# Performance work log

Measured on AMD Instinct MI355X. Metric: run time of the kernel, lower is better.

The kernel has to match this reference:

```python
import jax, jax.numpy as jnp
import numpy as np

B, N, C, H, BS = 4, 4096, 1024, 16, 64
E = C // H          # head dim = 64
EPS = 1e-3

def setup_inputs() -> dict:
    key = jax.random.key(0)
    k0, k1, k2, k3 = jax.random.split(key, 4)
    x = jax.random.normal(k0, (B, N, C), jnp.float32)
    qkv_w = jax.random.normal(k1, (3 * C, C), jnp.float32) * 0.02
    proj_w = jax.random.normal(k2, (C, C), jnp.float32) * 0.02
    proj_b = jax.random.normal(k3, (C,), jnp.float32) * 0.02
    return {"x": x, "qkv_w": qkv_w, "proj_w": proj_w, "proj_b": proj_b}

def reference(x, qkv_w, proj_w, proj_b):
    b, n, c = x.shape
    h, e, bs = H, E, BS
    u = n // bs  # number of buckets
    # qkv projection (no bias), split to (B,H,N,e) per q/k/v
    qkv = (x @ qkv_w.T).reshape(b, n, 3, h, e).transpose(2, 0, 3, 1, 4)
    q, k, v = qkv[0], qkv[1], qkv[2]
    # feature maps: softmax(q) scaled, exp(k)
    q = jax.nn.softmax(q, axis=-1) * (e ** -0.5)
    k = jnp.exp(k)
    # bucket along sequence: (B,H,U,BS,e)
    b_q = q.reshape(b, h, u, bs, e)
    b_k = k.reshape(b, h, u, bs, e)
    b_v = v.reshape(b, h, u, bs, e)
    # per-bucket k sums and inter-bucket cumulative sums
    b_k_cumsum = jnp.cumsum(b_k.sum(axis=-2), axis=-2)            # (B,H,U,e)
    context = jnp.einsum('bhund,bhune->bhude', b_k, b_v)          # (B,H,U,e,e)
    context = jnp.cumsum(context, axis=2)
    # exclusive shift by one bucket (bucket_size > 1 path in original)
    context = jnp.concatenate(
        [jnp.zeros_like(context[:, :, :1]), context[:, :, :-1]], axis=2)
    b_k_cumsum = jnp.concatenate(
        [jnp.zeros_like(b_k_cumsum[:, :, :1]), b_k_cumsum[:, :, :-1]], axis=2)
    # normalizer, clamped from below at eps
    D_inv = 1.0 / jnp.maximum(
        jnp.einsum('bhud,bhund->bhun', b_k_cumsum, b_q), EPS)
    attn = jnp.einsum('bhund,bhude,bhun->bhune', b_q, context, D_inv)
    out = attn.reshape(b, h, n, e).transpose(0, 2, 1, 3).reshape(b, n, c)
    # output projection (dropouts are identity at eval)
    return out @ proj_w.T + proj_b
```

## Files before the change

kernel.cpp:

```cpp
#include <hip/hip_runtime.h>
#include <stdint.h>


typedef unsigned short u16;
typedef unsigned int u32;
typedef u16   u16x4  __attribute__((ext_vector_type(4)));
typedef u16   u16x8  __attribute__((ext_vector_type(8)));
typedef float f32x4  __attribute__((ext_vector_type(4)));
typedef float float4v __attribute__((ext_vector_type(4)));
typedef __bf16 bf16x8 __attribute__((ext_vector_type(8)));

__device__ __forceinline__ u16 f2bf(float f) {
  return __builtin_bit_cast(u16, (__bf16)f);
}
__device__ __forceinline__ float bf2f(u16 h) {
  return (float)__builtin_bit_cast(__bf16, h);
}

__device__ __forceinline__ void stage16(const u16* g, u16* l) {
  __builtin_amdgcn_global_load_lds(
      (const __attribute__((address_space(1))) u32*)g,
      (__attribute__((address_space(3))) u32*)l, 16, 0, 0);
}

__global__ __launch_bounds__(256) void cvt_all(
    const float* __restrict__ x, const float* __restrict__ wqf,
    const float* __restrict__ wpf, u16* __restrict__ xb,
    u16* __restrict__ wq, u16* __restrict__ wp) {
  int i = blockIdx.x * 256 + threadIdx.x;
  const float* in; u16* out; int j;
  if (i < 4194304)      { in = x;   out = xb; j = i; }
  else if (i < 4980736) { in = wqf; out = wq; j = i - 4194304; }
  else                  { in = wpf; out = wp; j = i - 4980736; }
  float4v v = reinterpret_cast<const float4v*>(in)[j];
  u16x4 o;
  o.x = f2bf(v.x); o.y = f2bf(v.y); o.z = f2bf(v.z); o.w = f2bf(v.w);
  reinterpret_cast<u16x4*>(out)[j] = o;
}

template <int EPI>
__global__ __launch_bounds__(512, 2) void gemm256(
    const u16* __restrict__ A,
    const u16* __restrict__ B,
    const float* __restrict__ bias,
    float* __restrict__ Cf,
    u16* __restrict__ Qf, u16* __restrict__ Kr, u16* __restrict__ Vr,
    int N, int K, int NT) {
  __shared__ u16 As[2][2][256][32];
  __shared__ u16 Bs[2][2][256][32];
  const int tid = threadIdx.x, lane = tid & 63, wave = tid >> 6;
  const int wm = wave >> 2, wn = wave & 3;
  const int l15 = lane & 15, l4 = lane >> 4;
  const int ntn = N >> 8;
  const int cpx = gridDim.x >> 3;
  const int bid = (blockIdx.x & 7) * cpx + (blockIdx.x >> 3);
  const int bm = bid / ntn, bn = bid % ntn;

  const int srow = tid >> 2;
  const int gsl8 = ((tid & 3) ^ ((tid >> 3) & 3)) * 8;
  const u16* Ag = A + (size_t)(bm * 256 + srow) * K + gsl8;
  const u16* Bg = B + (size_t)(bn * 256 + srow) * K + gsl8;
  const size_t rj = (size_t)128 * K;

  const int slotr = (l4 ^ ((l15 >> 1) & 3)) * 8;

  f32x4 acc[8][4] = {};
  bf16x8 a0, a1, a2, a3, a4, a5, a6, a7, b0, b1, b2, b3;

#define STG(P, buf, kh, kt)                                        \
  { const u16* g_ = P##g + (kt) + (kh) * 32;                       \
    stage16(g_,      &P##s[buf][kh][wave * 16][0]);                \
    stage16(g_ + rj, &P##s[buf][kh][128 + wave * 16][0]); }

#define LDA(r0_, r1_, r2_, r3_, kk, mh)                                  \
  { const u16* p_ = &As[cur][kk][wm * 128 + (mh) * 64 + l15][0] + slotr; \
    r0_ = *(const bf16x8*)(p_);                                          \
    r1_ = *(const bf16x8*)(p_ + 512);                                    \
    r2_ = *(const bf16x8*)(p_ + 1024);                                   \
    r3_ = *(const bf16x8*)(p_ + 1536); }

#define LDB(kk)                                                    \
  { const u16* p_ = &Bs[cur][kk][wn * 64 + l15][0] + slotr;        \
    b0 = *(const bf16x8*)(p_);                                     \
    b1 = *(const bf16x8*)(p_ + 512);                               \
    b2 = *(const bf16x8*)(p_ + 1024);                              \
    b3 = *(const bf16x8*)(p_ + 1536); }

#define MM(x, y, z) z = __builtin_amdgcn_mfma_f32_16x16x32_bf16(x, y, z, 0, 0, 0)
#define MFMA16(mb, x0, x1, x2, x3)                                 \
  __builtin_amdgcn_s_setprio(1);                                   \
  MM(x0, b0, acc[(mb) + 0][0]); MM(x0, b1, acc[(mb) + 0][1]);      \
  MM(x0, b2, acc[(mb) + 0][2]); MM(x0, b3, acc[(mb) + 0][3]);      \
  MM(x1, b0, acc[(mb) + 1][0]); MM(x1, b1, acc[(mb) + 1][1]);      \
  MM(x1, b2, acc[(mb) + 1][2]); MM(x1, b3, acc[(mb) + 1][3]);      \
  MM(x2, b0, acc[(mb) + 2][0]); MM(x2, b1, acc[(mb) + 2][1]);      \
  MM(x2, b2, acc[(mb) + 2][2]); MM(x2, b3, acc[(mb) + 2][3]);      \
  MM(x3, b0, acc[(mb) + 3][0]); MM(x3, b1, acc[(mb) + 3][1]);      \
  MM(x3, b2, acc[(mb) + 3][2]); MM(x3, b3, acc[(mb) + 3][3]);      \
  __builtin_amdgcn_s_setprio(0);

#define BARF()                                                     \
  { asm volatile("" ::: "memory");                                 \
    __builtin_amdgcn_s_barrier();                                  \
    asm volatile("" ::: "memory"); }

  STG(A, 0, 0, 0) STG(B, 0, 0, 0) STG(A, 0, 1, 0) STG(B, 0, 1, 0)
  asm volatile("s_waitcnt vmcnt(0)" ::: "memory");
  __builtin_amdgcn_s_barrier();
  asm volatile("" ::: "memory");

  for (int t = 0; t < NT; ++t) {
    const int cur = t & 1, nxt = cur ^ 1;
    const int ktn = (t + 1) << 6;
    const bool pre = (t + 1 < NT);
    LDB(0)
    LDA(a0, a1, a2, a3, 0, 0)
    LDA(a4, a5, a6, a7, 0, 1)
    if (pre) STG(A, nxt, 0, ktn)
    MFMA16(0, a0, a1, a2, a3)
    if (pre) STG(B, nxt, 0, ktn)
    MFMA16(4, a4, a5, a6, a7)
    if (pre) { asm volatile("s_waitcnt vmcnt(4)" ::: "memory"); }
    else     { asm volatile("s_waitcnt vmcnt(0)" ::: "memory"); }
    BARF()
    LDB(1)
    LDA(a0, a1, a2, a3, 1, 0)
    LDA(a4, a5, a6, a7, 1, 1)
    if (pre) STG(A, nxt, 1, ktn)
    MFMA16(0, a0, a1, a2, a3)
    if (pre) STG(B, nxt, 1, ktn)
    MFMA16(4, a4, a5, a6, a7)
    if (pre) { asm volatile("s_waitcnt vmcnt(4)" ::: "memory"); }
    BARF()
  }
#undef STG
#undef LDA
#undef LDB
#undef MM
#undef MFMA16
#undef BARF

  const int row0 = bm * 256 + wm * 128 + l4 * 4;
  const int col0 = bn * 256 + wn * 64 + l15;
  if constexpr (EPI == 0) {
    float bv[4];
#pragma unroll
    for (int ni = 0; ni < 4; ++ni) bv[ni] = bias[col0 + ni * 16];
#pragma unroll
    for (int mi = 0; mi < 8; ++mi)
#pragma unroll
      for (int i = 0; i < 4; ++i) {
        size_t r = (size_t)(row0 + mi * 16 + i) * N;
#pragma unroll
        for (int ni = 0; ni < 4; ++ni)
          Cf[r + col0 + ni * 16] = acc[mi][ni][i] + bv[ni];
      }
  } else {
    const int i3 = bn >> 2;
    const int h  = ((bn & 3) << 2) + wn;
    u16* dst = (i3 == 0) ? Qf : (i3 == 1 ? Kr : Vr);
#pragma unroll
    for (int mi = 0; mi < 8; ++mi)
#pragma unroll
      for (int i = 0; i < 4; ++i) {
        const int row = row0 + mi * 16 + i;
        const int bb = row >> 12, uu = (row >> 6) & 63, nn = row & 63;
        u16* op = dst + ((size_t)((bb * 16 + h) * 64 + uu)) * 4096
                      + nn * 64 + l15;
        float v0 = acc[mi][0][i], v1 = acc[mi][1][i];
        float v2 = acc[mi][2][i], v3 = acc[mi][3][i];
        if (i3 == 0) {
          float mx = fmaxf(fmaxf(v0, v1), fmaxf(v2, v3));
          mx = fmaxf(mx, __shfl_xor(mx, 1));
          mx = fmaxf(mx, __shfl_xor(mx, 2));
          mx = fmaxf(mx, __shfl_xor(mx, 4));
          mx = fmaxf(mx, __shfl_xor(mx, 8));
          float e0 = __expf(v0 - mx), e1 = __expf(v1 - mx);
          float e2 = __expf(v2 - mx), e3 = __expf(v3 - mx);
          float s = e0 + e1 + e2 + e3;
          s += __shfl_xor(s, 1); s += __shfl_xor(s, 2);
          s += __shfl_xor(s, 4); s += __shfl_xor(s, 8);
          float inv = 0.125f / s;
          op[0]  = f2bf(e0 * inv); op[16] = f2bf(e1 * inv);
          op[32] = f2bf(e2 * inv); op[48] = f2bf(e3 * inv);
        } else if (i3 == 1) {
          op[0]  = f2bf(__expf(v0)); op[16] = f2bf(__expf(v1));
          op[32] = f2bf(__expf(v2)); op[48] = f2bf(__expf(v3));
        } else {
          op[0]  = f2bf(v0); op[16] = f2bf(v1);
          op[32] = f2bf(v2); op[48] = f2bf(v3);
        }
      }
  }
}

__global__ __launch_bounds__(256) void buildctx(
    const u16* __restrict__ Kr,
    const u16* __restrict__ Vr,
    u16* __restrict__ ctxb, float* __restrict__ ksum) {
  const int bid = blockIdx.x;
  const int tid = threadIdx.x, lane = tid & 63, wave = tid >> 6;
  const int l15 = lane & 15, l4 = lane >> 4;
  __shared__ float ts[64][65];
  __shared__ u16 KtL[64][72];
  __shared__ u16 VtL[64][72];
  __shared__ float dp[64][4];

  const size_t base = (size_t)bid * 4096;

  {
    int n = tid >> 2, c = tid & 3;
    const u16* kp = Kr + base + n * 64 + c * 16;
#pragma unroll
    for (int j = 0; j < 16; ++j) ts[n][c * 16 + j] = bf2f(kp[j]);
  }
  __syncthreads();
  {
    int d = tid >> 2, c = tid & 3;
    u16x8 o0, o1;
#pragma unroll
    for (int j = 0; j < 8; ++j) o0[j] = f2bf(ts[c * 16 + j][d]);
#pragma unroll
    for (int j = 0; j < 8; ++j) o1[j] = f2bf(ts[c * 16 + 8 + j][d]);
    *reinterpret_cast<u16x8*>(&KtL[d][c * 16])     = o0;
    *reinterpret_cast<u16x8*>(&KtL[d][c * 16 + 8]) = o1;
  }
  __syncthreads();
  {
    int d = tid & 63, q = tid >> 6;
    float a = 0.f;
#pragma unroll
    for (int j = 0; j < 16; ++j) a += bf2f(KtL[d][q * 16 + j]);
    dp[d][q] = a;
  }
  {
    int n = tid >> 2, c = tid & 3;
    const u16* vp = Vr + base + n * 64 + c * 16;
#pragma unroll
    for (int j = 0; j < 16; ++j) ts[n][c * 16 + j] = bf2f(vp[j]);
  }
  __syncthreads();
  if (tid < 64)
    ksum[(size_t)bid * 64 + tid] = dp[tid][0] + dp[tid][1] + dp[tid][2] + dp[tid][3];
  {
    int e = tid >> 2, c = tid & 3;
    u16x8 o0, o1;
#pragma unroll
    for (int j = 0; j < 8; ++j) o0[j] = f2bf(ts[c * 16 + j][e]);
#pragma unroll
    for (int j = 0; j < 8; ++j) o1[j] = f2bf(ts[c * 16 + 8 + j][e]);
    *reinterpret_cast<u16x8*>(&VtL[e][c * 16])     = o0;
    *reinterpret_cast<u16x8*>(&VtL[e][c * 16 + 8]) = o1;
  }
  __syncthreads();

  f32x4 acc[4] = {};
#pragma unroll
  for (int kk = 0; kk < 2; ++kk) {
    bf16x8 av = *reinterpret_cast<const bf16x8*>(&VtL[wave * 16 + l15][kk * 32 + l4 * 8]);
#pragma unroll
    for (int ni = 0; ni < 4; ++ni) {
      bf16x8 bk = *reinterpret_cast<const bf16x8*>(&KtL[ni * 16 + l15][kk * 32 + l4 * 8]);
      acc[ni] = __builtin_amdgcn_mfma_f32_16x16x32_bf16(av, bk, acc[ni], 0, 0, 0);
    }
  }
  u16* cb = ctxb + base;
#pragma unroll
  for (int ni = 0; ni < 4; ++ni)
#pragma unroll
    for (int i = 0; i < 4; ++i)
      cb[(wave * 16 + l4 * 4 + i) * 64 + ni * 16 + l15] = f2bf(acc[ni][i]);
}

__global__ __launch_bounds__(256) void scanctx(
    u16* __restrict__ ctxb, float* __restrict__ ksum) {
  const int bh = blockIdx.x >> 2, c = blockIdx.x & 3;
  const int tid = threadIdx.x;
  u16* p = ctxb + (size_t)bh * 64 * 4096 + c * 1024 + tid * 4;
  float* kp = ksum + (size_t)bh * 64 * 64 + tid;
  const bool dok = (c == 0) && (tid < 64);

  float r0 = 0.f, r1 = 0.f, r2 = 0.f, r3 = 0.f, runk = 0.f;
#define LC(i) (*reinterpret_cast<const u16x4*>(p + (size_t)(i) * 4096))
#define LK(i) (dok ? kp[(size_t)(i) * 64] : 0.f)
  u16x4 c0 = LC(0), c1 = LC(1), c2 = LC(2), c3 = LC(3);
  float k0 = LK(0), k1 = LK(1), k2 = LK(2), k3 = LK(3);
  for (int u = 0; u < 64; u += 4) {
    const int i4 = u + 4 < 64 ? u + 4 : 63, i5 = u + 5 < 64 ? u + 5 : 63;
    const int i6 = u + 6 < 64 ? u + 6 : 63, i7 = u + 7 < 64 ? u + 7 : 63;
    u16x4 n0 = LC(i4), n1 = LC(i5), n2 = LC(i6), n3 = LC(i7);
    float m0 = LK(i4), m1 = LK(i5), m2 = LK(i6), m3 = LK(i7);
#define STEP(idx, cv, kv)                                                  \
    {                                                                      \
      u16x4 o;                                                             \
      o.x = f2bf(r0); o.y = f2bf(r1); o.z = f2bf(r2); o.w = f2bf(r3);      \
      *reinterpret_cast<u16x4*>(p + (size_t)(idx) * 4096) = o;             \
      if (dok) kp[(size_t)(idx) * 64] = runk;                              \
      r0 += bf2f(cv.x); r1 += bf2f(cv.y); r2 += bf2f(cv.z);                \
      r3 += bf2f(cv.w); runk += kv;                                        \
    }
    STEP(u, c0, k0) STEP(u + 1, c1, k1) STEP(u + 2, c2, k2) STEP(u + 3, c3, k3)
#undef STEP
    c0 = n0; c1 = n1; c2 = n2; c3 = n3;
    k0 = m0; k1 = m1; k2 = m2; k3 = m3;
  }
#undef LC
#undef LK
}

__global__ __launch_bounds__(256) void apply(
    const u16* __restrict__ Q, const u16* __restrict__ ctxc,
    const float* __restrict__ kcum, u16* __restrict__ AT) {
  const int bid = blockIdx.x;
  const int u = bid & 63, bh = bid >> 6, b = bh >> 4, h = bh & 15;
  const int tid = threadIdx.x, lane = tid & 63, wave = tid >> 6;
  const int l15 = lane & 15, l4 = lane >> 4;
  __shared__ float kc[64];
  __shared__ float dp[64][4];
  __shared__ float dinv[64];

  const size_t base = (size_t)bid * 4096;
  const u16* Qu = Q + base;
  if (tid < 64) kc[tid] = kcum[(size_t)bid * 64 + tid];
  __syncthreads();
  {
    int n = tid & 63, q = tid >> 6;
    const u16* qp = Qu + n * 64 + q * 16;
    float a = 0.f;
#pragma unroll
    for (int j = 0; j < 16; ++j) a += bf2f(qp[j]) * kc[q * 16 + j];
    dp[n][q] = a;
  }
  __syncthreads();
  if (tid < 64)
    dinv[tid] = 1.f / fmaxf(dp[tid][0] + dp[tid][1] + dp[tid][2] + dp[tid][3], 1e-3f);
  __syncthreads();

  f32x4 acc[4] = {};
  const u16* Cu = ctxc + base;
#pragma unroll
  for (int kk = 0; kk < 2; ++kk) {
    bf16x8 aq = *reinterpret_cast<const bf16x8*>(Qu + (wave * 16 + l15) * 64 + kk * 32 + l4 * 8);
#pragma unroll
    for (int ni = 0; ni < 4; ++ni) {
      bf16x8 bc = *reinterpret_cast<const bf16x8*>(Cu + (ni * 16 + l15) * 64 + kk * 32 + l4 * 8);
      acc[ni] = __builtin_amdgcn_mfma_f32_16x16x32_bf16(aq, bc, acc[ni], 0, 0, 0);
    }
  }
  const size_t orow = ((size_t)b * 4096 + u * 64 + wave * 16 + l4 * 4) * 1024 + h * 64;
#pragma unroll
  for (int i = 0; i < 4; ++i) {
    float di = dinv[wave * 16 + l4 * 4 + i];
#pragma unroll
    for (int ni = 0; ni < 4; ++ni)
      AT[orow + (size_t)i * 1024 + ni * 16 + l15] = f2bf(acc[ni][i] * di);
  }
}

extern "C" void kernel_launch(void* const* d_in, const int* in_sizes, int n_in,
                              void* d_out, int out_size, void* d_ws, size_t ws_size,
                              hipStream_t stream) {
  (void)in_sizes; (void)n_in; (void)out_size; (void)ws_size;
  const float* x      = (const float*)d_in[0];
  const float* qkv_w  = (const float*)d_in[1];
  const float* proj_w = (const float*)d_in[2];
  const float* proj_b = (const float*)d_in[3];
  float* out = (float*)d_out;

  char* ws = (char*)d_ws;
  u16* xb    = (u16*)(ws);
  u16* wq    = (u16*)(ws + 33554432);
  u16* wp    = (u16*)(ws + 39845888);
  u16* Qf    = (u16*)(ws + 41943040);
  u16* Kr    = (u16*)(ws + 75497472);
  u16* Vr    = (u16*)(ws + 109051904);
  u16* ctxb  = (u16*)(ws + 142606336);
  float* ksum = (float*)(ws + 176160768);
  u16* AT    = Kr;

  cvt_all<<<dim3(20480), dim3(256), 0, stream>>>(x, qkv_w, proj_w, xb, wq, wp);

  gemm256<2><<<dim3(64 * 12), dim3(512), 0, stream>>>(
      xb, wq, nullptr, nullptr, Qf, Kr, Vr, 3072, 1024, 16);
  buildctx<<<dim3(4096), dim3(256), 0, stream>>>(Kr, Vr, ctxb, ksum);
  scanctx<<<dim3(256), dim3(256), 0, stream>>>(ctxb, ksum);
  apply<<<dim3(4096), dim3(256), 0, stream>>>(Qf, ctxb, ksum, AT);
  gemm256<0><<<dim3(64 * 4), dim3(512), 0, stream>>>(
      AT, wp, proj_b, out, nullptr, nullptr, nullptr, 1024, 1024, 16);
}
```

Measured before the change: 244.9 us.

## Write K and V transposed from QKV GEMM epilogue, drop LDS transposes in buildctx

The QKV GEMM epilogue now stores exp(K) and V per bucket in a transposed (d-major) layout, with each lane writing four consecutive sequence positions as one 8-byte store. buildctx then reads MFMA operands and key sums straight from global memory, with no LDS staging, transposes or the extra barriers that went with them. The cost moves into the epilogue, whose stores are now strided by 64 elements across lanes and may coalesce less well than the earlier row-major writes.

```diff
diff --git a/kernel.cpp b/kernel.cpp
--- a/kernel.cpp
+++ b/kernel.cpp
@@ -44,7 +44,7 @@
     const u16* __restrict__ B,
     const float* __restrict__ bias,
     float* __restrict__ Cf,
-    u16* __restrict__ Qf, u16* __restrict__ Kr, u16* __restrict__ Vr,
+    u16* __restrict__ Qf, u16* __restrict__ Kt, u16* __restrict__ Vt,
     int N, int K, int NT) {
   __shared__ u16 As[2][2][256][32];
   __shared__ u16 Bs[2][2][256][32];
@@ -158,18 +158,17 @@
   } else {
     const int i3 = bn >> 2;
     const int h  = ((bn & 3) << 2) + wn;
-    u16* dst = (i3 == 0) ? Qf : (i3 == 1 ? Kr : Vr);
-#pragma unroll
-    for (int mi = 0; mi < 8; ++mi)
-#pragma unroll
-      for (int i = 0; i < 4; ++i) {
-        const int row = row0 + mi * 16 + i;
-        const int bb = row >> 12, uu = (row >> 6) & 63, nn = row & 63;
-        u16* op = dst + ((size_t)((bb * 16 + h) * 64 + uu)) * 4096
-                      + nn * 64 + l15;
-        float v0 = acc[mi][0][i], v1 = acc[mi][1][i];
-        float v2 = acc[mi][2][i], v3 = acc[mi][3][i];
-        if (i3 == 0) {
+    if (i3 == 0) {
+#pragma unroll
+      for (int mi = 0; mi < 8; ++mi)
+#pragma unroll
+        for (int i = 0; i < 4; ++i) {
+          const int row = row0 + mi * 16 + i;
+          const int bb = row >> 12, uu = (row >> 6) & 63, nn = row & 63;
+          u16* op = Qf + ((size_t)((bb * 16 + h) * 64 + uu)) * 4096
+                        + nn * 64 + l15;
+          float v0 = acc[mi][0][i], v1 = acc[mi][1][i];
+          float v2 = acc[mi][2][i], v3 = acc[mi][3][i];
           float mx = fmaxf(fmaxf(v0, v1), fmaxf(v2, v3));
           mx = fmaxf(mx, __shfl_xor(mx, 1));
           mx = fmaxf(mx, __shfl_xor(mx, 2));
@@ -183,87 +182,68 @@
           float inv = 0.125f / s;
           op[0]  = f2bf(e0 * inv); op[16] = f2bf(e1 * inv);
           op[32] = f2bf(e2 * inv); op[48] = f2bf(e3 * inv);
-        } else if (i3 == 1) {
-          op[0]  = f2bf(__expf(v0)); op[16] = f2bf(__expf(v1));
-          op[32] = f2bf(__expf(v2)); op[48] = f2bf(__expf(v3));
-        } else {
-          op[0]  = f2bf(v0); op[16] = f2bf(v1);
-          op[32] = f2bf(v2); op[48] = f2bf(v3);
+        }
+    } else {
+      u16* dst = (i3 == 1) ? Kt : Vt;
+#pragma unroll
+      for (int mi = 0; mi < 8; ++mi) {
+        const int row = row0 + mi * 16;
+        const int bb = row >> 12, uu = (row >> 6) & 63, nn = row & 63;
+        u16* op = dst + ((size_t)((bb * 16 + h) * 64 + uu)) * 4096 + nn;
+#pragma unroll
+        for (int ni = 0; ni < 4; ++ni) {
+          const int d = ni * 16 + l15;
+          u16x4 o;
+          if (i3 == 1) {
+            o.x = f2bf(__expf(acc[mi][ni][0]));
+            o.y = f2bf(__expf(acc[mi][ni][1]));
+            o.z = f2bf(__expf(acc[mi][ni][2]));
+            o.w = f2bf(__expf(acc[mi][ni][3]));
+          } else {
+            o.x = f2bf(acc[mi][ni][0]); o.y = f2bf(acc[mi][ni][1]);
+            o.z = f2bf(acc[mi][ni][2]); o.w = f2bf(acc[mi][ni][3]);
+          }
+          *reinterpret_cast<u16x4*>(op + d * 64) = o;
         }
       }
+    }
   }
 }
 
 __global__ __launch_bounds__(256) void buildctx(
-    const u16* __restrict__ Kr,
-    const u16* __restrict__ Vr,
+    const u16* __restrict__ Kt,
+    const u16* __restrict__ Vt,
     u16* __restrict__ ctxb, float* __restrict__ ksum) {
   const int bid = blockIdx.x;
   const int tid = threadIdx.x, lane = tid & 63, wave = tid >> 6;
   const int l15 = lane & 15, l4 = lane >> 4;
-  __shared__ float ts[64][65];
-  __shared__ u16 KtL[64][72];
-  __shared__ u16 VtL[64][72];
   __shared__ float dp[64][4];
-
   const size_t base = (size_t)bid * 4096;
 
-  {
-    int n = tid >> 2, c = tid & 3;
-    const u16* kp = Kr + base + n * 64 + c * 16;
-#pragma unroll
-    for (int j = 0; j < 16; ++j) ts[n][c * 16 + j] = bf2f(kp[j]);
-  }
-  __syncthreads();
   {
     int d = tid >> 2, c = tid & 3;
-    u16x8 o0, o1;
-#pragma unroll
-    for (int j = 0; j < 8; ++j) o0[j] = f2bf(ts[c * 16 + j][d]);
-#pragma unroll
-    for (int j = 0; j < 8; ++j) o1[j] = f2bf(ts[c * 16 + 8 + j][d]);
-    *reinterpret_cast<u16x8*>(&KtL[d][c * 16])     = o0;
-    *reinterpret_cast<u16x8*>(&KtL[d][c * 16 + 8]) = o1;
-  }
-  __syncthreads();
-  {
-    int d = tid & 63, q = tid >> 6;
+    const u16* kp = Kt + base + d * 64 + c * 16;
     float a = 0.f;
 #pragma unroll
-    for (int j = 0; j < 16; ++j) a += bf2f(KtL[d][q * 16 + j]);
-    dp[d][q] = a;
-  }
-  {
-    int n = tid >> 2, c = tid & 3;
-    const u16* vp = Vr + base + n * 64 + c * 16;
-#pragma unroll
-    for (int j = 0; j < 16; ++j) ts[n][c * 16 + j] = bf2f(vp[j]);
+    for (int j = 0; j < 16; ++j) a += bf2f(kp[j]);
+    dp[d][c] = a;
+  }
+
+  f32x4 acc[4] = {};
+#pragma unroll
+  for (int kk = 0; kk < 2; ++kk) {
+    bf16x8 av = *reinterpret_cast<const bf16x8*>(
+        Vt + base + (wave * 16 + l15) * 64 + kk * 32 + l4 * 8);
+#pragma unroll
+    for (int ni = 0; ni < 4; ++ni) {
+      bf16x8 bk = *reinterpret_cast<const bf16x8*>(
+          Kt + base + (ni * 16 + l15) * 64 + kk * 32 + l4 * 8);
+      acc[ni] = __builtin_amdgcn_mfma_f32_16x16x32_bf16(av, bk, acc[ni], 0, 0, 0);
+    }
   }
   __syncthreads();
   if (tid < 64)
     ksum[(size_t)bid * 64 + tid] = dp[tid][0] + dp[tid][1] + dp[tid][2] + dp[tid][3];
-  {
-    int e = tid >> 2, c = tid & 3;
-    u16x8 o0, o1;
-#pragma unroll
-    for (int j = 0; j < 8; ++j) o0[j] = f2bf(ts[c * 16 + j][e]);
-#pragma unroll
-    for (int j = 0; j < 8; ++j) o1[j] = f2bf(ts[c * 16 + 8 + j][e]);
-    *reinterpret_cast<u16x8*>(&VtL[e][c * 16])     = o0;
-    *reinterpret_cast<u16x8*>(&VtL[e][c * 16 + 8]) = o1;
-  }
-  __syncthreads();
-
-  f32x4 acc[4] = {};
-#pragma unroll
-  for (int kk = 0; kk < 2; ++kk) {
-    bf16x8 av = *reinterpret_cast<const bf16x8*>(&VtL[wave * 16 + l15][kk * 32 + l4 * 8]);
-#pragma unroll
-    for (int ni = 0; ni < 4; ++ni) {
-      bf16x8 bk = *reinterpret_cast<const bf16x8*>(&KtL[ni * 16 + l15][kk * 32 + l4 * 8]);
-      acc[ni] = __builtin_amdgcn_mfma_f32_16x16x32_bf16(av, bk, acc[ni], 0, 0, 0);
-    }
-  }
   u16* cb = ctxb + base;
 #pragma unroll
   for (int ni = 0; ni < 4; ++ni)
@@ -372,17 +352,17 @@
   u16* wq    = (u16*)(ws + 33554432);
   u16* wp    = (u16*)(ws + 39845888);
   u16* Qf    = (u16*)(ws + 41943040);
-  u16* Kr    = (u16*)(ws + 75497472);
-  u16* Vr    = (u16*)(ws + 109051904);
+  u16* Kt    = (u16*)(ws + 75497472);
+  u16* Vt    = (u16*)(ws + 109051904);
   u16* ctxb  = (u16*)(ws + 142606336);
   float* ksum = (float*)(ws + 176160768);
-  u16* AT    = Kr;
+  u16* AT    = Kt;
 
   cvt_all<<<dim3(20480), dim3(256), 0, stream>>>(x, qkv_w, proj_w, xb, wq, wp);
 
   gemm256<2><<<dim3(64 * 12), dim3(512), 0, stream>>>(
-      xb, wq, nullptr, nullptr, Qf, Kr, Vr, 3072, 1024, 16);
-  buildctx<<<dim3(4096), dim3(256), 0, stream>>>(Kr, Vr, ctxb, ksum);
+      xb, wq, nullptr, nullptr, Qf, Kt, Vt, 3072, 1024, 16);
+  buildctx<<<dim3(4096), dim3(256), 0, stream>>>(Kt, Vt, ctxb, ksum);
   scanctx<<<dim3(256), dim3(256), 0, stream>>>(ctxb, ksum);
   apply<<<dim3(4096), dim3(256), 0, stream>>>(Qf, ctxb, ksum, AT);
   gemm256<0><<<dim3(64 * 4), dim3(512), 0, stream>>>(
```

Measured after the change: 249.1 us. No clear change (+1.7%).
